# Kernel optimization log

Hardware: AMD Instinct MI355X
Metric: run time of the kernel (lower is better)

Reference implementation:

```python
import math
import jax, jax.numpy as jnp
import numpy as np

B, S, D, H = 2, 2048, 2048, 16
HD = D // H  # 128
EPS = 1e-5


def setup_inputs() -> dict:
    key = jax.random.key(0)
    ks = jax.random.split(key, 7)
    x = jax.random.normal(ks[0], (B, S, D), jnp.float32)
    # RoPE tables: (seqlen, head_dim//2)
    theta = 10000.0
    inv_freq = 1.0 / (theta ** (np.arange(0, HD, 2, dtype=np.float32) / HD))
    t = np.arange(S, dtype=np.float32)
    freqs = np.outer(t, inv_freq)  # (S, HD//2)
    freqs_cos = jnp.asarray(np.cos(freqs), jnp.float32)
    freqs_sin = jnp.asarray(np.sin(freqs), jnp.float32)
    sc = 0.02
    wq = jax.random.normal(ks[1], (D, D), jnp.float32) * sc  # stored (in, out)
    wk = jax.random.normal(ks[2], (D, D), jnp.float32) * sc
    wv = jax.random.normal(ks[3], (D, D), jnp.float32) * sc
    wu = jax.random.normal(ks[4], (D, D), jnp.float32) * sc
    wo = jax.random.normal(ks[5], (D, D), jnp.float32) * sc
    norm_w = jnp.ones((D,), jnp.float32)
    return {"x": x, "freqs_cos": freqs_cos, "freqs_sin": freqs_sin,
            "wq": wq, "wk": wk, "wv": wv, "wu": wu, "wo": wo, "norm_w": norm_w}


def _rope(t, cos, sin):
    # t: (B, S, H, HD); cos/sin: (S, HD//2)
    tr = t.reshape(t.shape[:-1] + (-1, 2))
    r, i = tr[..., 0], tr[..., 1]
    c = cos[None, :, None, :]
    s = sin[None, :, None, :]
    out_r = r * c - i * s
    out_i = r * s + i * c
    return jnp.stack([out_r, out_i], axis=-1).reshape(t.shape)


def reference(x, freqs_cos, freqs_sin, wq, wk, wv, wu, wo, norm_w):
    b, s, d = x.shape
    h = jax.nn.silu(x)  # pre-projection SiLU on the input
    q = (h @ wq).reshape(b, s, H, HD)
    k = (h @ wk).reshape(b, s, H, HD)
    v = (h @ wv).reshape(b, s, H, HD)
    u = h @ wu  # reshape->transpose->flatten in original is identity on (b,s,d)
    q = _rope(q, freqs_cos, freqs_sin)
    k = _rope(k, freqs_cos, freqs_sin)
    # scores: (b, H, s, s)
    scores = jnp.einsum('bqhd,bkhd->bhqk', q, k) / math.sqrt(HD)
    causal = jnp.tril(jnp.ones((s, s), bool))  # mask!=0 positions zeroed; silu(0)=0
    scores = jnp.where(causal[None, None], jax.nn.silu(scores), 0.0)
    out = jnp.einsum('bhqk,bkhd->bqhd', scores, v).reshape(b, s, d)
    # RMSNorm
    out = out * jax.lax.rsqrt(jnp.mean(out * out, axis=-1, keepdims=True) + EPS)
    out = out * norm_w
    out = out * u
    return out @ wo
```

## Files before the change

### kernel.cpp

```cpp
#include <hip/hip_runtime.h>
#include <hip/hip_bf16.h>
#include <cstdint>

typedef __attribute__((ext_vector_type(8))) short bf16x8;
typedef __attribute__((ext_vector_type(4))) float f32x4;
typedef unsigned short u16;

constexpr int B = 2, S = 2048, D = 2048, H = 16, HD = 128;
constexpr int M = B * S;
constexpr int NQKU = 6144;
constexpr int ATT_LD = 3072;
constexpr float SCALE = 0.08838834764831845f;

static __device__ __forceinline__ float b2f(u16 u) {
    union { float f; uint32_t i; } v; v.i = ((uint32_t)u) << 16; return v.f;
}
static __device__ __forceinline__ u16 f2b(float f) {
    union { float f; uint32_t i; } v; v.f = f;
    uint32_t x = v.i;
    return (u16)((x + 0x7FFFu + ((x >> 16) & 1u)) >> 16);
}

__device__ __forceinline__ void gll16(const void* g, void* l) {
    __builtin_amdgcn_global_load_lds(
        (const __attribute__((address_space(1))) uint32_t*)g,
        (__attribute__((address_space(3))) uint32_t*)l, 16, 0, 0);
}

#define BAR() do { asm volatile("" ::: "memory"); __builtin_amdgcn_s_barrier(); \
                   asm volatile("" ::: "memory"); } while (0)

__global__ __launch_bounds__(256) void silu_cast(const float* __restrict__ x,
                                                 u16* __restrict__ h, int n) {
    int i = (blockIdx.x * 256 + threadIdx.x) * 4;
    if (i >= n) return;
    float4 v = *(const float4*)(x + i);
    ushort4 o;
    o.x = f2b(v.x / (1.f + __expf(-v.x)));
    o.y = f2b(v.y / (1.f + __expf(-v.y)));
    o.z = f2b(v.z / (1.f + __expf(-v.z)));
    o.w = f2b(v.w / (1.f + __expf(-v.w)));
    *(ushort4*)(h + i) = o;
}

__global__ __launch_bounds__(256) void wcast(const float* __restrict__ w,
                                             u16* __restrict__ wT) {
    __shared__ float t[64][65];
    int tx = threadIdx.x & 63, ty = threadIdx.x >> 6;
    int kb = blockIdx.y * 64, nb = blockIdx.x * 64;
    for (int r = ty; r < 64; r += 4)
        t[r][tx] = w[(size_t)(kb + r) * D + nb + tx];
    __syncthreads();
    for (int r = ty; r < 64; r += 4)
        wT[(size_t)(nb + r) * D + kb + tx] = f2b(t[tx][r]);
}

__global__ __launch_bounds__(512, 2)
void gemm_qkuv(const u16* __restrict__ A, const u16* __restrict__ BT,
               u16* __restrict__ qku, u16* __restrict__ vt) {
    __shared__ u16 lds[65536];
    const int tid = threadIdx.x;
    const int lane = tid & 63, wid = tid >> 6;
    const int wm = wid >> 2, wn = wid & 3;
    const int l16 = lane & 15, lq = lane >> 4;

    const int orig = blockIdx.x;
    const int swz = (orig & 7) * 64 + (orig >> 3);
    const int mt = swz & 15, nt = swz >> 4;
    const int m0 = mt * 256, n0 = nt * 256;

    const int srow = tid >> 2;
    const int ce = ((tid & 3) * 8) ^ (((tid >> 5) & 1) << 4);
    const int rdx = (lq * 16) ^ (((l16 >> 3) & 1) << 5);

    const u16* As0 = A + (size_t)(m0 + srow) * D + ce;
    const u16* Bs0 = BT + (size_t)(n0 + srow) * D + ce;

    {
        u16* dA = lds + wid * 512;
        u16* dB = lds + 16384 + wid * 512;
        gll16(As0,                    dA);
        gll16(As0 + (size_t)128 * D,  dA + 8192);
        gll16(Bs0,                    dB);
        gll16(Bs0 + (size_t)128 * D,  dB + 8192);
        gll16(As0 + 32,                    dA + 4096);
        gll16(As0 + 32 + (size_t)128 * D,  dA + 8192 + 4096);
        gll16(Bs0 + 32,                    dB + 4096);
        gll16(Bs0 + 32 + (size_t)128 * D,  dB + 8192 + 4096);
    }
    asm volatile("s_waitcnt vmcnt(4)" ::: "memory");
    BAR();

    f32x4 acc[8][4] = {};
    bf16x8 a[8];
    const int rbB = (wn & 1) * 4096;

#define LOAD_A(kk)                                                            \
    _Pragma("unroll") for (int mi = 0; mi < 8; ++mi)                          \
        a[mi] = *(const bf16x8*)(Abase + (kk) * 8192 +                        \
                                 (mi * 16 + l16) * 64 + rdx);
#define LOAD_B(dst, nia, kk)                                                  \
    dst = *(const bf16x8*)(Bbase + (kk) * 8192 + rbB +                        \
                           ((nia) * 16 + l16) * 64 + rdx);
#define MFMA2(n0i, n1i)                                                       \
    __builtin_amdgcn_s_setprio(1);                                            \
    _Pragma("unroll") for (int mi = 0; mi < 8; ++mi) {                        \
        acc[mi][n0i] = __builtin_amdgcn_mfma_f32_16x16x32_bf16(a[mi], b0,     \
                            acc[mi][n0i], 0, 0, 0);                           \
        acc[mi][n1i] = __builtin_amdgcn_mfma_f32_16x16x32_bf16(a[mi], b1,     \
                            acc[mi][n1i], 0, 0, 0);                           \
    }                                                                          \
    __builtin_amdgcn_s_setprio(0);

    for (int kt = 0; kt < 32; ++kt) {
        const int buf = kt & 1;
        const char* Abase = (const char*)lds + buf * 65536 + wm * 16384;
        const char* Bbase = (const char*)lds + 32768 + buf * 65536 + (wn >> 1) * 16384;
        const bool st = (kt + 1) < 32;
        const u16* Asrc = As0 + (kt + 1) * 64;
        const u16* Bsrc = Bs0 + (kt + 1) * 64;
        u16* dA = lds + (buf ^ 1) * 32768 + wid * 512;
        u16* dB = dA + 16384;
        bf16x8 b0, b1;

        LOAD_A(0);
        LOAD_B(b0, 0, 0);
        LOAD_B(b1, 1, 0);
        if (st) { gll16(Asrc, dA); gll16(Asrc + (size_t)128 * D, dA + 8192); }
        BAR();
        MFMA2(0, 1);
        BAR();
        LOAD_B(b0, 2, 0);
        LOAD_B(b1, 3, 0);
        if (st) { gll16(Bsrc, dB); gll16(Bsrc + (size_t)128 * D, dB + 8192); }
        BAR();
        MFMA2(2, 3);
        if (kt == 31) asm volatile("s_waitcnt vmcnt(0)" ::: "memory");
        else         asm volatile("s_waitcnt vmcnt(4)" ::: "memory");
        BAR();
        LOAD_A(1);
        LOAD_B(b0, 0, 1);
        LOAD_B(b1, 1, 1);
        if (st) { gll16(Asrc + 32, dA + 4096); gll16(Asrc + 32 + (size_t)128 * D, dA + 8192 + 4096); }
        BAR();
        MFMA2(0, 1);
        BAR();
        LOAD_B(b0, 2, 1);
        LOAD_B(b1, 3, 1);
        if (st) { gll16(Bsrc + 32, dB + 4096); gll16(Bsrc + 32 + (size_t)128 * D, dB + 8192 + 4096); }
        BAR();
        MFMA2(2, 3);
        if (kt < 31) asm volatile("s_waitcnt vmcnt(4)" ::: "memory");
        BAR();
    }
#undef LOAD_A
#undef LOAD_B
#undef MFMA2

    if (n0 >= NQKU) {
#pragma unroll
        for (int mi = 0; mi < 8; ++mi)
#pragma unroll
            for (int ni = 0; ni < 4; ++ni) {
                int c = n0 - NQKU + wn * 64 + ni * 16 + l16;
                int hh = c >> 7, d = c & 127;
                int row0 = m0 + wm * 128 + mi * 16 + lq * 4;
                int bb = row0 >> 11, s0 = row0 & 2047;
                ushort4 pk = make_ushort4(f2b(acc[mi][ni][0]), f2b(acc[mi][ni][1]),
                                          f2b(acc[mi][ni][2]), f2b(acc[mi][ni][3]));
                *(ushort4*)(vt + (((size_t)(bb * H + hh) * HD + d) * S + s0)) = pk;
            }
    } else {
#pragma unroll
        for (int mi = 0; mi < 8; ++mi)
#pragma unroll
            for (int ni = 0; ni < 4; ++ni)
#pragma unroll
                for (int r = 0; r < 4; ++r) {
                    int row = m0 + wm * 128 + mi * 16 + lq * 4 + r;
                    int col = n0 + wn * 64 + ni * 16 + l16;
                    qku[(size_t)row * NQKU + col] = f2b(acc[mi][ni][r]);
                }
    }
}

__global__ __launch_bounds__(256)
void gemm_bt_f32(const u16* __restrict__ A, const u16* __restrict__ BT,
                 float* __restrict__ out, int lda, int ldc, int Kk) {
    __shared__ u16 As[128 * 32];
    __shared__ u16 Bs[128 * 32];
    const int tid = threadIdx.x;
    const int lane = tid & 63, w = tid >> 6;
    const int wm = w >> 1, wn = w & 1;
    const int l16 = lane & 15, lq = lane >> 4;
    const int m0 = blockIdx.y * 128, n0 = blockIdx.x * 128;
    const int rs = lane >> 2;
    const int cs = (lane & 3) * 8;
    f32x4 acc[4][4] = {};

    const u16* Ab = A + (size_t)(m0 + w * 32 + rs) * lda + cs;
    const u16* Bb = BT + (size_t)(n0 + w * 32 + rs) * Kk + cs;
    u16* Al = As + w * 32 * 32;
    u16* Bl = Bs + w * 32 * 32;

    for (int k0 = 0; k0 < Kk; k0 += 32) {
        gll16(Ab + k0, Al);
        gll16(Ab + k0 + (size_t)16 * lda, Al + 16 * 32);
        gll16(Bb + k0, Bl);
        gll16(Bb + k0 + (size_t)16 * Kk, Bl + 16 * 32);
        __syncthreads();
        bf16x8 af[4], bfr[4];
#pragma unroll
        for (int mi = 0; mi < 4; mi++)
            af[mi] = *(const bf16x8*)(As + (wm * 64 + mi * 16 + l16) * 32 + lq * 8);
#pragma unroll
        for (int ni = 0; ni < 4; ni++)
            bfr[ni] = *(const bf16x8*)(Bs + (wn * 64 + ni * 16 + l16) * 32 + lq * 8);
#pragma unroll
        for (int mi = 0; mi < 4; mi++)
#pragma unroll
            for (int ni = 0; ni < 4; ni++)
                acc[mi][ni] = __builtin_amdgcn_mfma_f32_16x16x32_bf16(
                    af[mi], bfr[ni], acc[mi][ni], 0, 0, 0);
        __syncthreads();
    }
#pragma unroll
    for (int mi = 0; mi < 4; mi++)
#pragma unroll
        for (int ni = 0; ni < 4; ni++)
#pragma unroll
            for (int r = 0; r < 4; r++) {
                int row = m0 + wm * 64 + mi * 16 + lq * 4 + r;
                int col = n0 + wn * 64 + ni * 16 + l16;
                out[(size_t)row * ldc + col] = acc[mi][ni][r];
            }
}

__global__ __launch_bounds__(256)
void reformat(const u16* __restrict__ qku, const float* __restrict__ fc,
              const float* __restrict__ fs, u16* __restrict__ qr,
              u16* __restrict__ kr) {
    int bh = blockIdx.x;
    int s0 = blockIdx.y * 64;
    int b = bh >> 4, h = bh & 15;
    int tid = threadIdx.x;
#pragma unroll
    for (int i = 0; i < 16; ++i) {
        int p = tid + i * 256;
        int row = p >> 6, pp = p & 63;
        int sgl = s0 + row;
        float c = fc[sgl * 64 + pp], sn = fs[sgl * 64 + pp];
        size_t src = (size_t)(b * S + sgl) * NQKU + h * HD + 2 * pp;
        size_t dst = ((size_t)bh * S + sgl) * HD + 2 * pp;
        {
            uint32_t qv = *(const uint32_t*)(qku + src);
            float r = b2f((u16)(qv & 0xffff)), im = b2f((u16)(qv >> 16));
            uint32_t o = (uint32_t)f2b(r * c - im * sn) |
                         ((uint32_t)f2b(r * sn + im * c) << 16);
            *(uint32_t*)(qr + dst) = o;
        }
        {
            uint32_t kv = *(const uint32_t*)(qku + src + 2048);
            float r = b2f((u16)(kv & 0xffff)), im = b2f((u16)(kv >> 16));
            uint32_t o = (uint32_t)f2b(r * c - im * sn) |
                         ((uint32_t)f2b(r * sn + im * c) << 16);
            *(uint32_t*)(kr + dst) = o;
        }
    }
}

__global__ __launch_bounds__(512, 2)
void hstu_attn(const u16* __restrict__ qr, const u16* __restrict__ kr,
               const u16* __restrict__ vt, float* __restrict__ att) {
    __shared__ u16 k_l[16384];
    __shared__ u16 v_l[16384];
    __shared__ u16 s_l[128 * 136];
    const int bh = blockIdx.x & 31, slot = blockIdx.x >> 5;
    const int b = bh >> 4, h = bh & 15;
    const int tid = threadIdx.x, lane = tid & 63, w = tid >> 6;
    const int l16 = lane & 15, lq = lane >> 4;
    const int wq = w >> 2, wk4 = w & 3;

    const u16* kb = kr + (size_t)bh * S * HD;
    const u16* vb = vt + (size_t)bh * HD * S;
    const int irow0 = tid >> 4, iu0 = tid & 15;

#define STAGE_K(k0_)                                                          \
    _Pragma("unroll") for (int r_ = 0; r_ < 4; ++r_) {                        \
        int row_ = irow0 + r_ * 32;                                           \
        int uc_ = iu0 ^ (row_ & 7);                                           \
        gll16(kb + (size_t)(k0_ + row_) * HD + uc_ * 8,                       \
              k_l + ((w * 64 + r_ * 512) << 3));                              \
    }
#define STAGE_V(k0_)                                                          \
    _Pragma("unroll") for (int r_ = 0; r_ < 4; ++r_) {                        \
        int row_ = irow0 + r_ * 32;                                           \
        int uc_ = iu0 ^ (row_ & 7);                                           \
        gll16(vb + (size_t)row_ * S + (k0_) + uc_ * 8,                        \
              v_l + ((w * 64 + r_ * 512) << 3));                              \
    }

    for (int pass = 0; pass < 2; ++pass) {
        const int t = pass ? (15 - slot) : slot;
        const int q0 = t * 128;

        bf16x8 qf[4][4];
#pragma unroll
        for (int mi = 0; mi < 4; ++mi)
#pragma unroll
            for (int kk = 0; kk < 4; ++kk)
                qf[mi][kk] = *(const bf16x8*)(qr +
                    ((size_t)bh * S + q0 + wq * 64 + mi * 16 + l16) * HD +
                    kk * 32 + lq * 8);
        f32x4 acco[4][2] = {};

        STAGE_K(0);
        STAGE_V(0);
        asm volatile("s_waitcnt vmcnt(0)" ::: "memory");
        BAR();

        for (int kt = 0; kt <= t; ++kt) {
            const int k0 = kt * 128;
            const bool st = kt < t;
            f32x4 accs[4][2] = {};
            __builtin_amdgcn_s_setprio(1);
#pragma unroll
            for (int kk = 0; kk < 4; ++kk)
#pragma unroll
                for (int ni = 0; ni < 2; ++ni) {
                    int row = wk4 * 32 + ni * 16 + l16;
                    bf16x8 kf = *(const bf16x8*)(k_l + row * 128 +
                                ((kk * 32 + lq * 8) ^ ((row & 7) << 3)));
#pragma unroll
                    for (int mi = 0; mi < 4; ++mi)
                        accs[mi][ni] = __builtin_amdgcn_mfma_f32_16x16x32_bf16(
                            qf[mi][kk], kf, accs[mi][ni], 0, 0, 0);
                }
            __builtin_amdgcn_s_setprio(0);
            const bool dg = (kt == t);
#pragma unroll
            for (int mi = 0; mi < 4; ++mi)
#pragma unroll
                for (int ni = 0; ni < 2; ++ni)
#pragma unroll
                    for (int r = 0; r < 4; ++r) {
                        int qrow = wq * 64 + mi * 16 + lq * 4 + r;
                        int krow = wk4 * 32 + ni * 16 + l16;
                        float vv = accs[mi][ni][r] * SCALE;
                        vv = (!dg || (k0 + krow <= q0 + qrow))
                                 ? vv * __builtin_amdgcn_rcpf(1.f + __expf(-vv))
                                 : 0.f;
                        s_l[qrow * 136 + krow] = f2b(vv);
                    }
            BAR();
            if (st) STAGE_K(k0 + 128);
            if (st) asm volatile("s_waitcnt vmcnt(4)" ::: "memory");
            else    asm volatile("s_waitcnt vmcnt(0)" ::: "memory");
            BAR();
            __builtin_amdgcn_s_setprio(1);
#pragma unroll
            for (int kk = 0; kk < 4; ++kk) {
                bf16x8 sf[4];
#pragma unroll
                for (int mi = 0; mi < 4; ++mi)
                    sf[mi] = *(const bf16x8*)(s_l + (wq * 64 + mi * 16 + l16) * 136 +
                                              kk * 32 + lq * 8);
#pragma unroll
                for (int ni = 0; ni < 2; ++ni) {
                    int row = wk4 * 32 + ni * 16 + l16;
                    bf16x8 vf = *(const bf16x8*)(v_l + row * 128 +
                                ((kk * 32 + lq * 8) ^ ((row & 7) << 3)));
#pragma unroll
                    for (int mi = 0; mi < 4; ++mi)
                        acco[mi][ni] = __builtin_amdgcn_mfma_f32_16x16x32_bf16(
                            sf[mi], vf, acco[mi][ni], 0, 0, 0);
                }
            }
            __builtin_amdgcn_s_setprio(0);
            BAR();
            if (st) {
                STAGE_V(k0 + 128);
                asm volatile("s_waitcnt vmcnt(4)" ::: "memory");
            }
            BAR();
        }
#pragma unroll
        for (int mi = 0; mi < 4; ++mi)
#pragma unroll
            for (int ni = 0; ni < 2; ++ni)
#pragma unroll
                for (int r = 0; r < 4; ++r)
                    att[(size_t)(b * S + q0 + wq * 64 + mi * 16 + lq * 4 + r) * ATT_LD +
                        h * HD + wk4 * 32 + ni * 16 + l16] = acco[mi][ni][r];
    }
#undef STAGE_K
#undef STAGE_V
}

__global__ __launch_bounds__(256)
void rms_mul(const float* __restrict__ att, u16* __restrict__ qku,
             const float* __restrict__ nw) {
    int row = blockIdx.x;
    int tid = threadIdx.x;
    const float* a = att + (size_t)row * ATT_LD + tid * 8;
    float4 v0 = *(const float4*)(a);
    float4 v1 = *(const float4*)(a + 4);
    float ss = v0.x * v0.x + v0.y * v0.y + v0.z * v0.z + v0.w * v0.w +
               v1.x * v1.x + v1.y * v1.y + v1.z * v1.z + v1.w * v1.w;
#pragma unroll
    for (int off = 32; off > 0; off >>= 1) ss += __shfl_down(ss, off, 64);
    __shared__ float red[4];
    int lane = tid & 63, w = tid >> 6;
    if (lane == 0) red[w] = ss;
    __syncthreads();
    float rs = rsqrtf((red[0] + red[1] + red[2] + red[3]) * (1.f / D) + 1e-5f);
    int col = tid * 8;
    u16* up = qku + (size_t)row * NQKU + 4096 + col;
    u16 ut[8];
    *(int4*)ut = *(const int4*)up;
    float f[8] = {v0.x, v0.y, v0.z, v0.w, v1.x, v1.y, v1.z, v1.w};
    u16 o[8];
#pragma unroll
    for (int j = 0; j < 8; j++)
        o[j] = f2b(f[j] * rs * nw[col + j] * b2f(ut[j]));
    *(int4*)up = *(int4*)o;
}

extern "C" void kernel_launch(void* const* d_in, const int* in_sizes, int n_in,
                              void* d_out, int out_size, void* d_ws, size_t ws_size,
                              hipStream_t stream) {
    const float* x  = (const float*)d_in[0];
    const float* fc = (const float*)d_in[1];
    const float* fs = (const float*)d_in[2];
    const float* wq = (const float*)d_in[3];
    const float* wk = (const float*)d_in[4];
    const float* wv = (const float*)d_in[5];
    const float* wu = (const float*)d_in[6];
    const float* wo = (const float*)d_in[7];
    const float* nw = (const float*)d_in[8];
    float* out = (float*)d_out;

    char* ws = (char*)d_ws;
    const size_t WSZ = (size_t)D * D * sizeof(u16);
    u16* h_b  = (u16*)(ws);
    u16* wT   = (u16*)(ws + 2 * WSZ);
    u16* qku  = (u16*)(ws + 7 * WSZ);
    u16* vt   = (u16*)(ws + 13 * WSZ);
    u16* k_r  = (u16*)(ws + 15 * WSZ);
    u16* q_r  = h_b;
    float* att = (float*)qku;

    silu_cast<<<M * D / 1024, 256, 0, stream>>>(x, h_b, M * D);
    dim3 wg(32, 32);
    wcast<<<wg, 256, 0, stream>>>(wq, wT + 0 * (size_t)D * D);
    wcast<<<wg, 256, 0, stream>>>(wk, wT + 1 * (size_t)D * D);
    wcast<<<wg, 256, 0, stream>>>(wu, wT + 2 * (size_t)D * D);
    wcast<<<wg, 256, 0, stream>>>(wv, wT + 3 * (size_t)D * D);
    wcast<<<wg, 256, 0, stream>>>(wo, wT + 4 * (size_t)D * D);

    gemm_qkuv<<<512, 512, 0, stream>>>(h_b, wT, qku, vt);

    reformat<<<dim3(32, 32), 256, 0, stream>>>(qku, fc, fs, q_r, k_r);
    hstu_attn<<<256, 512, 0, stream>>>(q_r, k_r, vt, att);
    rms_mul<<<M, 256, 0, stream>>>(att, qku, nw);
    gemm_bt_f32<<<dim3(D / 128, M / 128), 256, 0, stream>>>(
        qku + 4096, wT + 4 * (size_t)D * D, out, NQKU, D, D);
}
```

Baseline: 342.5 us.

## Split causal attention work evenly across twice as many blocks with atomic merge

Attention is rebuilt to use 64-wide key tiles and 512 blocks. Each block handles exactly 17 key tiles from a pair of query tiles (short and long), which balances the causal triangle. The second query tile is shared by two blocks, so its output is combined with atomicAdd into a buffer zeroed by a new kernel. Smaller LDS tiles allow four blocks per CU instead of two. The cost is an extra zeroing launch, atomic float adds with order-dependent rounding, and more loop bookkeeping per iteration.

After: 481.1 us. +40.4%, slower.

```diff
diff --git a/kernel.cpp b/kernel.cpp
--- a/kernel.cpp
+++ b/kernel.cpp
@@ -269,132 +269,170 @@
     }
 }
 
-__global__ __launch_bounds__(512, 2)
+__global__ __launch_bounds__(256) void zero_att(float* __restrict__ att) {
+    int row = blockIdx.x;
+    int b_ = row >> 10, q = 1024 + (row & 1023);
+    float* p = att + (size_t)(b_ * S + q) * ATT_LD;
+    float4 z = {0.f, 0.f, 0.f, 0.f};
+    *(float4*)(p + threadIdx.x * 4) = z;
+    *(float4*)(p + (threadIdx.x + 256) * 4) = z;
+}
+
+__global__ __launch_bounds__(512, 4)
 void hstu_attn(const u16* __restrict__ qr, const u16* __restrict__ kr,
                const u16* __restrict__ vt, float* __restrict__ att) {
-    __shared__ u16 k_l[16384];
-    __shared__ u16 v_l[16384];
-    __shared__ u16 s_l[128 * 136];
-    const int bh = blockIdx.x & 31, slot = blockIdx.x >> 5;
+    __shared__ u16 k_l[64 * 128];
+    __shared__ u16 v_l[128 * 64];
+    __shared__ u16 s_l[128 * 72];
+
+    const int id = blockIdx.x;
+    const int bh = (id & 7) * 4 + ((id >> 3) >> 4);
+    const int rem = (id >> 3) & 15;
+    const int p = rem >> 1, c = rem & 1;
     const int b = bh >> 4, h = bh & 15;
     const int tid = threadIdx.x, lane = tid & 63, w = tid >> 6;
     const int l16 = lane & 15, lq = lane >> 4;
-    const int wq = w >> 2, wk4 = w & 3;
+    const int wq = w >> 1, wk2 = w & 1;
 
     const u16* kb = kr + (size_t)bh * S * HD;
     const u16* vb = vt + (size_t)bh * HD * S;
-    const int irow0 = tid >> 4, iu0 = tid & 15;
-
-#define STAGE_K(k0_)                                                          \
-    _Pragma("unroll") for (int r_ = 0; r_ < 4; ++r_) {                        \
-        int row_ = irow0 + r_ * 32;                                           \
-        int uc_ = iu0 ^ (row_ & 7);                                           \
-        gll16(kb + (size_t)(k0_ + row_) * HD + uc_ * 8,                       \
-              k_l + ((w * 64 + r_ * 512) << 3));                              \
-    }
-#define STAGE_V(k0_)                                                          \
-    _Pragma("unroll") for (int r_ = 0; r_ < 4; ++r_) {                        \
-        int row_ = irow0 + r_ * 32;                                           \
-        int uc_ = iu0 ^ (row_ & 7);                                           \
-        gll16(vb + (size_t)row_ * S + (k0_) + uc_ * 8,                        \
-              v_l + ((w * 64 + r_ * 512) << 3));                              \
-    }
-
-    for (int pass = 0; pass < 2; ++pass) {
-        const int t = pass ? (15 - slot) : slot;
+    const u16* qb = qr + (size_t)bh * S * HD;
+
+    const int tA = p, tB = 15 - p, nA = 2 * p + 2;
+    const int g0 = 17 * c, g1 = g0 + 17;
+    int t  = (g0 < nA) ? tA : tB;
+    int kt = (g0 < nA) ? g0 : g0 - nA;
+
+#define STAGE_K(k0_) do {                                                     \
+    _Pragma("unroll") for (int r_ = 0; r_ < 2; ++r_) {                        \
+        int i_ = tid + r_ * 512;                                              \
+        int row_ = i_ >> 4, iu_ = i_ & 15;                                    \
+        int uc_ = iu_ ^ (row_ & 7);                                           \
+        gll16(kb + (size_t)((k0_) + row_) * HD + uc_ * 8,                     \
+              k_l + (w * 64 + r_ * 512) * 8);                                 \
+    } } while (0)
+#define STAGE_V(k0_) do {                                                     \
+    _Pragma("unroll") for (int r_ = 0; r_ < 2; ++r_) {                        \
+        int i_ = tid + r_ * 512;                                              \
+        int d_ = i_ >> 3, iu_ = i_ & 7;                                       \
+        int uc_ = iu_ ^ (d_ & 7);                                             \
+        gll16(vb + (size_t)d_ * S + (k0_) + uc_ * 8,                          \
+              v_l + (w * 64 + r_ * 512) * 8);                                 \
+    } } while (0)
+#define LOAD_QF(t_) do {                                                      \
+    _Pragma("unroll") for (int mi_ = 0; mi_ < 2; ++mi_)                       \
+        _Pragma("unroll") for (int kk_ = 0; kk_ < 4; ++kk_)                   \
+            qf[mi_][kk_] = *(const bf16x8*)(qb +                              \
+                (size_t)((t_) * 128 + wq * 32 + mi_ * 16 + l16) * HD +        \
+                kk_ * 32 + lq * 8);                                           \
+    } while (0)
+
+    bf16x8 qf[2][4];
+    f32x4 acco[2][4] = {};
+    LOAD_QF(t);
+    STAGE_K(kt * 64);
+    STAGE_V(kt * 64);
+    asm volatile("s_waitcnt vmcnt(0)" ::: "memory");
+    BAR();
+
+    for (int g = g0; g < g1; ++g) {
+        const bool last = (g == g1 - 1);
+        const int gn = g + 1;
+        const int tn = (gn < nA) ? tA : tB;
+        const int ktn = (gn < nA) ? gn : gn - nA;
+        const bool sw = (!last) && (tn != t);
+        const int k0 = kt * 64;
         const int q0 = t * 128;
 
-        bf16x8 qf[4][4];
-#pragma unroll
-        for (int mi = 0; mi < 4; ++mi)
-#pragma unroll
-            for (int kk = 0; kk < 4; ++kk)
-                qf[mi][kk] = *(const bf16x8*)(qr +
-                    ((size_t)bh * S + q0 + wq * 64 + mi * 16 + l16) * HD +
-                    kk * 32 + lq * 8);
-        f32x4 acco[4][2] = {};
-
-        STAGE_K(0);
-        STAGE_V(0);
-        asm volatile("s_waitcnt vmcnt(0)" ::: "memory");
-        BAR();
-
-        for (int kt = 0; kt <= t; ++kt) {
-            const int k0 = kt * 128;
-            const bool st = kt < t;
-            f32x4 accs[4][2] = {};
-            __builtin_amdgcn_s_setprio(1);
-#pragma unroll
-            for (int kk = 0; kk < 4; ++kk)
-#pragma unroll
-                for (int ni = 0; ni < 2; ++ni) {
-                    int row = wk4 * 32 + ni * 16 + l16;
-                    bf16x8 kf = *(const bf16x8*)(k_l + row * 128 +
-                                ((kk * 32 + lq * 8) ^ ((row & 7) << 3)));
-#pragma unroll
-                    for (int mi = 0; mi < 4; ++mi)
-                        accs[mi][ni] = __builtin_amdgcn_mfma_f32_16x16x32_bf16(
-                            qf[mi][kk], kf, accs[mi][ni], 0, 0, 0);
+        f32x4 accs[2][2] = {};
+        __builtin_amdgcn_s_setprio(1);
+#pragma unroll
+        for (int kk = 0; kk < 4; ++kk)
+#pragma unroll
+            for (int ni = 0; ni < 2; ++ni) {
+                int row = wk2 * 32 + ni * 16 + l16;
+                bf16x8 kf = *(const bf16x8*)(k_l + row * 128 +
+                            ((kk * 32 + lq * 8) ^ ((row & 7) << 3)));
+#pragma unroll
+                for (int mi = 0; mi < 2; ++mi)
+                    accs[mi][ni] = __builtin_amdgcn_mfma_f32_16x16x32_bf16(
+                        qf[mi][kk], kf, accs[mi][ni], 0, 0, 0);
+            }
+        __builtin_amdgcn_s_setprio(0);
+        const bool dg = (kt >= 2 * t);
+#pragma unroll
+        for (int mi = 0; mi < 2; ++mi)
+#pragma unroll
+            for (int ni = 0; ni < 2; ++ni)
+#pragma unroll
+                for (int r = 0; r < 4; ++r) {
+                    int qrow = wq * 32 + mi * 16 + lq * 4 + r;
+                    int krow = wk2 * 32 + ni * 16 + l16;
+                    float vv = accs[mi][ni][r] * SCALE;
+                    vv = (!dg || (k0 + krow <= q0 + qrow))
+                             ? vv * __builtin_amdgcn_rcpf(1.f + __expf(-vv))
+                             : 0.f;
+                    s_l[qrow * 72 + krow] = f2b(vv);
                 }
-            __builtin_amdgcn_s_setprio(0);
-            const bool dg = (kt == t);
-#pragma unroll
-            for (int mi = 0; mi < 4; ++mi)
-#pragma unroll
-                for (int ni = 0; ni < 2; ++ni)
-#pragma unroll
-                    for (int r = 0; r < 4; ++r) {
-                        int qrow = wq * 64 + mi * 16 + lq * 4 + r;
-                        int krow = wk4 * 32 + ni * 16 + l16;
-                        float vv = accs[mi][ni][r] * SCALE;
-                        vv = (!dg || (k0 + krow <= q0 + qrow))
-                                 ? vv * __builtin_amdgcn_rcpf(1.f + __expf(-vv))
-                                 : 0.f;
-                        s_l[qrow * 136 + krow] = f2b(vv);
-                    }
-            BAR();
-            if (st) STAGE_K(k0 + 128);
-            if (st) asm volatile("s_waitcnt vmcnt(4)" ::: "memory");
-            else    asm volatile("s_waitcnt vmcnt(0)" ::: "memory");
-            BAR();
-            __builtin_amdgcn_s_setprio(1);
-#pragma unroll
-            for (int kk = 0; kk < 4; ++kk) {
-                bf16x8 sf[4];
-#pragma unroll
-                for (int mi = 0; mi < 4; ++mi)
-                    sf[mi] = *(const bf16x8*)(s_l + (wq * 64 + mi * 16 + l16) * 136 +
-                                              kk * 32 + lq * 8);
-#pragma unroll
-                for (int ni = 0; ni < 2; ++ni) {
-                    int row = wk4 * 32 + ni * 16 + l16;
-                    bf16x8 vf = *(const bf16x8*)(v_l + row * 128 +
-                                ((kk * 32 + lq * 8) ^ ((row & 7) << 3)));
-#pragma unroll
-                    for (int mi = 0; mi < 4; ++mi)
-                        acco[mi][ni] = __builtin_amdgcn_mfma_f32_16x16x32_bf16(
-                            sf[mi], vf, acco[mi][ni], 0, 0, 0);
-                }
+        BAR();
+        if (!last) STAGE_K(ktn * 64);
+        if (last) asm volatile("s_waitcnt vmcnt(0)" ::: "memory");
+        else      asm volatile("s_waitcnt vmcnt(2)" ::: "memory");
+        BAR();
+        __builtin_amdgcn_s_setprio(1);
+#pragma unroll
+        for (int kk = 0; kk < 2; ++kk) {
+            bf16x8 sf[2];
+#pragma unroll
+            for (int mi = 0; mi < 2; ++mi)
+                sf[mi] = *(const bf16x8*)(s_l + (wq * 32 + mi * 16 + l16) * 72 +
+                                          kk * 32 + lq * 8);
+#pragma unroll
+            for (int ni = 0; ni < 4; ++ni) {
+                int row = wk2 * 64 + ni * 16 + l16;
+                bf16x8 vf = *(const bf16x8*)(v_l + row * 64 +
+                            (((kk * 4 + lq) ^ (row & 7)) << 3));
+#pragma unroll
+                for (int mi = 0; mi < 2; ++mi)
+                    acco[mi][ni] = __builtin_amdgcn_mfma_f32_16x16x32_bf16(
+                        sf[mi], vf, acco[mi][ni], 0, 0, 0);
             }
-            __builtin_amdgcn_s_setprio(0);
-            BAR();
-            if (st) {
-                STAGE_V(k0 + 128);
-                asm volatile("s_waitcnt vmcnt(4)" ::: "memory");
+        }
+        __builtin_amdgcn_s_setprio(0);
+        BAR();
+        if (!last) {
+            STAGE_V(ktn * 64);
+            if (sw) {
+#pragma unroll
+                for (int mi = 0; mi < 2; ++mi)
+#pragma unroll
+                    for (int ni = 0; ni < 4; ++ni)
+#pragma unroll
+                        for (int r = 0; r < 4; ++r) {
+                            att[(size_t)(b * S + q0 + wq * 32 + mi * 16 + lq * 4 + r) * ATT_LD +
+                                h * HD + wk2 * 64 + ni * 16 + l16] = acco[mi][ni][r];
+                            acco[mi][ni][r] = 0.f;
+                        }
+                LOAD_QF(tB);
+                asm volatile("s_waitcnt vmcnt(0)" ::: "memory");
+            } else {
+                asm volatile("s_waitcnt vmcnt(2)" ::: "memory");
             }
             BAR();
         }
-#pragma unroll
-        for (int mi = 0; mi < 4; ++mi)
-#pragma unroll
-            for (int ni = 0; ni < 2; ++ni)
-#pragma unroll
-                for (int r = 0; r < 4; ++r)
-                    att[(size_t)(b * S + q0 + wq * 64 + mi * 16 + lq * 4 + r) * ATT_LD +
-                        h * HD + wk4 * 32 + ni * 16 + l16] = acco[mi][ni][r];
+        t = tn; kt = ktn;
     }
+#pragma unroll
+    for (int mi = 0; mi < 2; ++mi)
+#pragma unroll
+        for (int ni = 0; ni < 4; ++ni)
+#pragma unroll
+            for (int r = 0; r < 4; ++r)
+                atomicAdd(&att[(size_t)(b * S + tB * 128 + wq * 32 + mi * 16 + lq * 4 + r) * ATT_LD +
+                               h * HD + wk2 * 64 + ni * 16 + l16], acco[mi][ni][r]);
 #undef STAGE_K
 #undef STAGE_V
+#undef LOAD_QF
 }
 
 __global__ __launch_bounds__(256)
@@ -461,7 +499,8 @@
     gemm_qkuv<<<512, 512, 0, stream>>>(h_b, wT, qku, vt);
 
     reformat<<<dim3(32, 32), 256, 0, stream>>>(qku, fc, fs, q_r, k_r);
-    hstu_attn<<<256, 512, 0, stream>>>(q_r, k_r, vt, att);
+    zero_att<<<2048, 256, 0, stream>>>(att);
+    hstu_attn<<<512, 512, 0, stream>>>(q_r, k_r, vt, att);
     rms_mul<<<M, 256, 0, stream>>>(att, qku, nw);
     gemm_bt_f32<<<dim3(D / 128, M / 128), 256, 0, stream>>>(
         qku + 4096, wT + 4 * (size_t)D * D, out, NQKU, D, D);
```
